# Kernel optimization log

Measured on AMD Instinct MI355X. Metric: run time of the kernel, lower is better.

Reference implementation:

```python
import jax, jax.numpy as jnp
import numpy as np

NUM_ROUTING = 3

def squash(s):
    # squash along the unit_size axis (axis=2), exactly as the torch module
    mag_sq = jnp.sum(s * s, axis=2, keepdims=True)
    mag = jnp.sqrt(mag_sq)
    return mag_sq / (1.0 + mag_sq) * (s / mag)

def setup_inputs() -> dict:
    key = jax.random.key(0)
    k1, k2 = jax.random.split(key)
    B, in_unit, in_channel = 512, 8, 1152
    num_unit, unit_size = 10, 16
    x = jax.random.normal(k1, (B, in_unit, in_channel), dtype=jnp.float32)
    weight = jax.random.normal(k2, (in_channel, num_unit, unit_size, in_unit), dtype=jnp.float32)
    return {"x": x, "weight": weight}

def reference(x, weight):
    B = x.shape[0]
    C, J = weight.shape[0], weight.shape[1]  # in_channel, num_unit
    xt = jnp.swapaxes(x, 1, 2)  # [B, C, in_unit]
    # u_hat[c, j, b, s] = W[c, j, s, :] @ x[b, c, :]
    u_hat = jnp.einsum('cjsi,bci->cjbs', weight, xt)  # [C, J, B, S]
    b_ij = jnp.zeros((C, J), dtype=x.dtype)
    v = None
    for _ in range(NUM_ROUTING):
        # DGL degree-bucketing puts all J capsule nodes in one bucket, so the
        # softmax(dim=0) in capsule_reduce is over the num_unit axis per input capsule
        c = jax.nn.softmax(b_ij, axis=1)          # [C, J]
        s = jnp.einsum('cj,cjbs->jbs', c, u_hat)  # [J, B, S]
        v = squash(s)                             # [J, B, S]
        # update_edge: b_ij += mean over batch of <v_j, u_hat_ij>
        b_ij = b_ij + jnp.einsum('jbs,cjbs->cj', v, u_hat) / B
    # [J, B, S] -> [B, J, S] -> unsqueeze(1).unsqueeze(4).squeeze(1) -> [B, J, S, 1]
    return jnp.transpose(v, (1, 0, 2))[..., None]
```

## Files before the change

kernel.cpp:

```cpp
#include <hip/hip_runtime.h>
#include <math.h>

#define B_  512
#define I_  8
#define C_  1152
#define J_  10
#define S_  16
#define K1  9216
#define NKB 288
#define KBT 16

typedef short short8 __attribute__((ext_vector_type(8)));
typedef float floatx4 __attribute__((ext_vector_type(4)));

__device__ inline unsigned short f2bf(float f) {
    unsigned int u = __float_as_uint(f);
    return (unsigned short)((u + 0x7FFFu + ((u >> 16) & 1u)) >> 16);
}
__device__ inline unsigned int pack2(float a, float b) {
    return (unsigned int)f2bf(a) | ((unsigned int)f2bf(b) << 16);
}

__global__ __launch_bounds__(512) void k_pack(const float* __restrict__ x,
                                              const float* __restrict__ W,
                                              uint4* __restrict__ Bs,
                                              uint4* __restrict__ Bt,
                                              uint4* __restrict__ Wf,
                                              unsigned short* __restrict__ W2,
                                              float* __restrict__ b_ij) {
    __shared__ float lds[10240];
    const int task = blockIdx.x;
    const int t = threadIdx.x;
    const int w = t >> 6, L = t & 63, quad = L >> 4;

    if (task < 576) {
        const int bt = task / 36, kt = task % 36;
        const int b0 = bt * 32, k0 = kt * 256;
        #pragma unroll
        for (int p = 0; p < 4; p++) {
            int f4 = p * 512 + t;
            int row = f4 >> 6, c4 = (f4 & 63) << 2;
            *(float4*)&lds[row * 260 + c4] =
                *(const float4*)&x[(size_t)(b0 + row) * K1 + k0 + c4];
        }
        __syncthreads();
        #pragma unroll
        for (int p = 0; p < 2; p++) {
            const int bl = p * 16 + (L & 15);
            const float* s = &lds[bl * 260 + w * 32 + quad * 8];
            uint4 o;
            o.x = pack2(s[0], s[1]); o.y = pack2(s[2], s[3]);
            o.z = pack2(s[4], s[5]); o.w = pack2(s[6], s[7]);
            Bs[((size_t)(bt * 2 + p) * NKB + kt * 8 + w) * 64 + L] = o;
        }
        #pragma unroll
        for (int p = 0; p < 2; p++) {
            const int ntl = w * 2 + p;
            const int nl = ntl * 16 + (L & 15);
            float v[8];
            #pragma unroll
            for (int e = 0; e < 8; e++) v[e] = lds[(quad * 8 + e) * 260 + nl];
            uint4 o;
            o.x = pack2(v[0], v[1]); o.y = pack2(v[2], v[3]);
            o.z = pack2(v[4], v[5]); o.w = pack2(v[6], v[7]);
            Bt[((size_t)(kt * 16 + ntl) * KBT + bt) * 64 + L] = o;
        }
    } else if (task < 720) {
        const int c0 = (task - 576) * 8;
        #pragma unroll
        for (int p = 0; p < 5; p++) {
            int f4 = p * 512 + t;
            int cc = f4 / 320, off4 = (f4 % 320) << 2;
            *(float4*)&lds[cc * 1280 + off4] =
                *(const float4*)&W[(size_t)(c0 + cc) * 1280 + off4];
        }
        __syncthreads();
        #pragma unroll
        for (int p = 0; p < 3; p++) {
            int o = p * 512 + t;
            if (o < 1280) {
                int j = o >> 7, i = (o >> 4) & 7, m = o & 15;
                int k0w = i * C_ + c0;
                int Lw = m | (((k0w >> 3) & 3) << 4);
                float v[8];
                #pragma unroll
                for (int e = 0; e < 8; e++)
                    v[e] = lds[e * 1280 + j * 128 + m * 8 + i];
                uint4 og;
                og.x = pack2(v[0], v[1]); og.y = pack2(v[2], v[3]);
                og.z = pack2(v[4], v[5]); og.w = pack2(v[6], v[7]);
                Wf[((size_t)j * NKB + (k0w >> 5)) * 64 + Lw] = og;
            }
        }
        #pragma unroll
        for (int p = 0; p < 2; p++) {
            int o = p * 512 + t;
            if (o < 640) {
                int j = o >> 6, i = (o >> 3) & 7, cc = o & 7;
                unsigned int r8[8];
                #pragma unroll
                for (int h = 0; h < 8; h++)
                    r8[h] = pack2(lds[cc * 1280 + j * 128 + (2 * h) * 8 + i],
                                  lds[cc * 1280 + j * 128 + (2 * h + 1) * 8 + i]);
                unsigned short* dst = W2 + ((size_t)(j * 8 + i) * C_ + c0 + cc) * 16;
                *(uint4*)dst       = make_uint4(r8[0], r8[1], r8[2], r8[3]);
                *(uint4*)(dst + 8) = make_uint4(r8[4], r8[5], r8[6], r8[7]);
            }
        }
    } else {
        for (int idx = t; idx < C_ * J_; idx += 512) b_ij[idx] = 0.0f;
    }
}

__global__ __launch_bounds__(256) void k_sgemm_f(const short8* __restrict__ Wf,
                                                 const short8* __restrict__ Bs,
                                                 const float* __restrict__ b_ij,
                                                 unsigned short* __restrict__ Vf,
                                                 float* __restrict__ out,
                                                 int mode) {
    __shared__ float sm[1152 + 2048];
    const int t = threadIdx.x, w = t >> 6, L = t & 63, quad = L >> 4;
    const int j = blockIdx.x >> 4;
    const int ntp = blockIdx.x & 15;

    if (mode) {
        for (int c = t; c < C_; c += 256) {
            float bv[J_], mx = -1e30f;
            #pragma unroll
            for (int jj = 0; jj < J_; jj++) {
                bv[jj] = b_ij[c * J_ + jj]; mx = fmaxf(mx, bv[jj]);
            }
            float sum = 0.0f;
            #pragma unroll
            for (int jj = 0; jj < J_; jj++) sum += __expf(bv[jj] - mx);
            sm[c] = __expf(bv[j] - mx) / sum;
        }
    }
    __syncthreads();

    const short8* pA  = Wf + ((size_t)j * NKB + w * 72) * 64 + L;
    const short8* pB0 = Bs + ((size_t)(ntp * 2) * NKB + w * 72) * 64 + L;
    const short8* pB1 = pB0 + (size_t)NKB * 64;
    floatx4 c0 = {0.f, 0.f, 0.f, 0.f}, c1 = c0;

    if (mode) {
        #pragma unroll 1
        for (int half = 0; half < 2; half++) {
            #pragma unroll 4
            for (int ii = 0; ii < 36; ii++) {
                const int i = half * 36 + ii;
                short8 a = pA[i * 64];
                const int cb = ii * 32 + quad * 8;
                float4 cl = *(const float4*)&sm[cb];
                float4 ch = *(const float4*)&sm[cb + 4];
                float cn8[8] = {cl.x, cl.y, cl.z, cl.w, ch.x, ch.y, ch.z, ch.w};
                unsigned int* au = (unsigned int*)&a;
                short8 a2;
                unsigned int* ao = (unsigned int*)&a2;
                #pragma unroll
                for (int h = 0; h < 4; h++) {
                    float f0 = __uint_as_float(au[h] << 16)         * cn8[2 * h];
                    float f1 = __uint_as_float(au[h] & 0xffff0000u) * cn8[2 * h + 1];
                    ao[h] = pack2(f0, f1);
                }
                c0 = __builtin_amdgcn_mfma_f32_16x16x32_bf16(a2, pB0[i * 64], c0, 0, 0, 0);
                c1 = __builtin_amdgcn_mfma_f32_16x16x32_bf16(a2, pB1[i * 64], c1, 0, 0, 0);
            }
        }
    } else {
        #pragma unroll 4
        for (int i = 0; i < 72; i++) {
            short8 a = pA[i * 64];
            c0 = __builtin_amdgcn_mfma_f32_16x16x32_bf16(a, pB0[i * 64], c0, 0, 0, 0);
            c1 = __builtin_amdgcn_mfma_f32_16x16x32_bf16(a, pB1[i * 64], c1, 0, 0, 0);
        }
    }

    const int col = L & 15, rw = quad << 2;
    float* base = &sm[1152 + w * 512];
    #pragma unroll
    for (int r = 0; r < 4; r++) {
        base[      (rw + r) * 16 + col] = c0[r];
        base[256 + (rw + r) * 16 + col] = c1[r];
    }
    __syncthreads();

    if (t < 32) {
        const int ntl = t >> 4, bl = t & 15;
        float sv[S_]; float msq = 0.f;
        #pragma unroll
        for (int s = 0; s < S_; s++) {
            float a = 0.f;
            #pragma unroll
            for (int w4 = 0; w4 < 4; w4++)
                a += sm[1152 + w4 * 512 + ntl * 256 + s * 16 + bl];
            if (mode == 0) a *= 0.1f;
            sv[s] = a; msq += a * a;
        }
        const float scale = msq / ((1.f + msq) * sqrtf(msq));
        const int b = ntp * 32 + t;
        if (mode < 2) {
            const int kb = b >> 5, lh = (b >> 3) & 3, e = b & 7;
            #pragma unroll
            for (int s = 0; s < S_; s++)
                Vf[((size_t)(j * KBT + kb) * 64 + (s | (lh << 4))) * 8 + e] =
                    f2bf(sv[s] * scale);
        } else {
            float o16[S_];
            #pragma unroll
            for (int s = 0; s < S_; s++) o16[s] = sv[s] * scale;
            float* dst = &out[((size_t)b * J_ + j) * S_];
            #pragma unroll
            for (int r4 = 0; r4 < 4; r4++)
                *(float4*)(dst + r4 * 4) = *(float4*)(o16 + r4 * 4);
        }
    }
}

__global__ __launch_bounds__(512) void k_tgemm_bup(const short8* __restrict__ Vf,
                                                   const short8* __restrict__ Bt,
                                                   const unsigned short* __restrict__ W2,
                                                   float* __restrict__ b_ij) {
    __shared__ float Tl[16 * 132];
    const int t = threadIdx.x, w = t >> 6, L = t & 63;
    const int j = blockIdx.y, ntg = blockIdx.x;
    const int nt = ntg * 8 + w;
    const short8* pA = Vf + (size_t)j * KBT * 64 + L;
    const short8* pB = Bt + (size_t)nt * KBT * 64 + L;
    floatx4 a = {0.f, 0.f, 0.f, 0.f};
    #pragma unroll
    for (int kb = 0; kb < KBT; kb++)
        a = __builtin_amdgcn_mfma_f32_16x16x32_bf16(pA[kb * 64], pB[kb * 64], a, 0, 0, 0);
    const int col = L & 15, rw = (L >> 4) << 2;
    #pragma unroll
    for (int r = 0; r < 4; r++)
        Tl[(rw + r) * 132 + w * 16 + col] = a[r];
    __syncthreads();
    if (t < 128) {
        const int n0 = ntg * 128;
        const int i = n0 / C_, c0 = n0 % C_;
        const int c = c0 + t;
        const unsigned short* wp = W2 + ((size_t)(j * 8 + i) * C_ + c) * 16;
        uint4 w0 = *(const uint4*)wp;
        uint4 w1 = *(const uint4*)(wp + 8);
        unsigned int uw[8] = {w0.x, w0.y, w0.z, w0.w, w1.x, w1.y, w1.z, w1.w};
        float sum = 0.f;
        #pragma unroll
        for (int h = 0; h < 8; h++) {
            sum += Tl[(2 * h) * 132 + t]     * __uint_as_float(uw[h] << 16);
            sum += Tl[(2 * h + 1) * 132 + t] * __uint_as_float(uw[h] & 0xffff0000u);
        }
        atomicAdd(&b_ij[c * J_ + j], sum * (1.0f / 512.f));
    }
}

extern "C" void kernel_launch(void* const* d_in, const int* in_sizes, int n_in,
                              void* d_out, int out_size, void* d_ws, size_t ws_size,
                              hipStream_t stream) {
    const float* x = (const float*)d_in[0];
    const float* W = (const float*)d_in[1];
    float* out = (float*)d_out;
    float* ws  = (float*)d_ws;

    float* Bs_f = ws;
    float* Bt_f = Bs_f + 2359296;
    float* Wf_f = Bt_f + 2359296;
    float* W2_f = Wf_f + 737280;
    float* Vf_f = W2_f + 737280;
    float* bij  = Vf_f + 40960;

    k_pack<<<721, 512, 0, stream>>>(x, W, (uint4*)Bs_f, (uint4*)Bt_f,
                                    (uint4*)Wf_f, (unsigned short*)W2_f, bij);

    k_sgemm_f<<<160, 256, 0, stream>>>((const short8*)Wf_f, (const short8*)Bs_f,
                                       bij, (unsigned short*)Vf_f, out, 0);
    k_tgemm_bup<<<dim3(72, 10), 512, 0, stream>>>(
        (const short8*)Vf_f, (const short8*)Bt_f, (const unsigned short*)W2_f, bij);

    k_sgemm_f<<<160, 256, 0, stream>>>((const short8*)Wf_f, (const short8*)Bs_f,
                                       bij, (unsigned short*)Vf_f, out, 1);
    k_tgemm_bup<<<dim3(72, 10), 512, 0, stream>>>(
        (const short8*)Vf_f, (const short8*)Bt_f, (const unsigned short*)W2_f, bij);

    k_sgemm_f<<<160, 256, 0, stream>>>((const short8*)Wf_f, (const short8*)Bs_f,
                                       bij, (unsigned short*)Vf_f, out, 2);
}
```

Baseline: 143.8 us.

## Fuse routing iterations into one persistent kernel with grid barriers

Replaces the five separate s-GEMM and t-GEMM/b-update launches with a single persistent kernel of 360 blocks. The blocks step through all routing phases and synchronise with a software grid barrier built on agent-scope atomics. The s-GEMM tiles are also re-split from 32 to 16 batch columns with 8 waves splitting K, which raises parallelism to 320 tasks. This removes launch gaps and gives more blocks in the first phase. In exchange it relies on all 360 blocks being co-resident, and the barrier uses a spin timeout that could silently break correctness if residency fails.

```diff
diff --git a/kernel.cpp b/kernel.cpp
--- a/kernel.cpp
+++ b/kernel.cpp
@@ -9,6 +9,8 @@
 #define K1  9216
 #define NKB 288
 #define KBT 16
+#define NBL 360
+#define NT  512
 
 typedef short short8 __attribute__((ext_vector_type(8)));
 typedef float floatx4 __attribute__((ext_vector_type(4)));
@@ -19,6 +21,27 @@
 }
 __device__ inline unsigned int pack2(float a, float b) {
     return (unsigned int)f2bf(a) | ((unsigned int)f2bf(b) << 16);
+}
+
+__device__ __forceinline__ void grid_bar(int* bar) {
+    __builtin_amdgcn_fence(__ATOMIC_RELEASE, "workgroup");
+    __syncthreads();
+    if (threadIdx.x == 0) {
+        int g = __hip_atomic_load(&bar[1], __ATOMIC_RELAXED, __HIP_MEMORY_SCOPE_AGENT);
+        int old = __hip_atomic_fetch_add(&bar[0], 1, __ATOMIC_RELAXED, __HIP_MEMORY_SCOPE_AGENT);
+        if (old == NBL - 1) {
+            __hip_atomic_store(&bar[0], 0, __ATOMIC_RELAXED, __HIP_MEMORY_SCOPE_AGENT);
+            __hip_atomic_store(&bar[1], g + 1, __ATOMIC_RELAXED, __HIP_MEMORY_SCOPE_AGENT);
+        } else {
+            int spins = 0;
+            while (__hip_atomic_load(&bar[1], __ATOMIC_RELAXED, __HIP_MEMORY_SCOPE_AGENT) == g) {
+                __builtin_amdgcn_s_sleep(1);
+                if (++spins > (1 << 20)) break;
+            }
+        }
+    }
+    __syncthreads();
+    __builtin_amdgcn_fence(__ATOMIC_ACQUIRE, "workgroup");
 }
 
 __global__ __launch_bounds__(512) void k_pack(const float* __restrict__ x,
@@ -27,7 +50,8 @@
                                               uint4* __restrict__ Bt,
                                               uint4* __restrict__ Wf,
                                               unsigned short* __restrict__ W2,
-                                              float* __restrict__ b_ij) {
+                                              float* __restrict__ b_ij,
+                                              int* __restrict__ bar) {
     __shared__ float lds[10240];
     const int task = blockIdx.x;
     const int t = threadIdx.x;
@@ -109,148 +133,153 @@
         }
     } else {
         for (int idx = t; idx < C_ * J_; idx += 512) b_ij[idx] = 0.0f;
+        if (t < 16) bar[t] = 0;
     }
 }
 
-__global__ __launch_bounds__(256) void k_sgemm_f(const short8* __restrict__ Wf,
-                                                 const short8* __restrict__ Bs,
-                                                 const float* __restrict__ b_ij,
-                                                 unsigned short* __restrict__ Vf,
-                                                 float* __restrict__ out,
-                                                 int mode) {
-    __shared__ float sm[1152 + 2048];
-    const int t = threadIdx.x, w = t >> 6, L = t & 63, quad = L >> 4;
-    const int j = blockIdx.x >> 4;
-    const int ntp = blockIdx.x & 15;
-
-    if (mode) {
-        for (int c = t; c < C_; c += 256) {
-            float bv[J_], mx = -1e30f;
+__global__ __launch_bounds__(NT, 4) void k_main(
+    const short8* __restrict__ Wf, const short8* __restrict__ Bs,
+    const short8* __restrict__ Bt, const unsigned short* __restrict__ W2,
+    unsigned int* __restrict__ Vf_dw, float* __restrict__ b_ij,
+    float* __restrict__ out, int* __restrict__ bar)
+{
+    __shared__ float smf[6400];
+    unsigned int* smu = (unsigned int*)smf;
+    const int bid = blockIdx.x, t = threadIdx.x;
+    const int w = t >> 6, L = t & 63, quad = L >> 4;
+
+    for (int it = 0; it < 3; it++) {
+        for (int task = bid; task < 320; task += NBL) {
+            __syncthreads();
+            const int j = task >> 5, nt = task & 31;
+            if (it > 0) {
+                for (int c = t; c < C_; c += NT) {
+                    float bv[J_], mx = -1e30f;
+                    #pragma unroll
+                    for (int jj = 0; jj < J_; jj++) {
+                        bv[jj] = __hip_atomic_load(&b_ij[c * J_ + jj],
+                                 __ATOMIC_RELAXED, __HIP_MEMORY_SCOPE_AGENT);
+                        mx = fmaxf(mx, bv[jj]);
+                    }
+                    float sum = 0.0f;
+                    #pragma unroll
+                    for (int jj = 0; jj < J_; jj++) sum += __expf(bv[jj] - mx);
+                    smf[c] = __expf(bv[j] - mx) / sum;
+                }
+            }
+            __syncthreads();
+            const short8* pA = Wf + ((size_t)j * NKB + w * 36) * 64 + L;
+            const short8* pB = Bs + ((size_t)nt * NKB + w * 36) * 64 + L;
+            floatx4 acc = {0.f, 0.f, 0.f, 0.f};
+            if (it > 0) {
+                #pragma unroll 4
+                for (int i = 0; i < 36; i++) {
+                    short8 a = pA[i * 64];
+                    const int cb = i * 32 + quad * 8;
+                    float4 cl = *(const float4*)&smf[cb];
+                    float4 ch = *(const float4*)&smf[cb + 4];
+                    float cn8[8] = {cl.x, cl.y, cl.z, cl.w, ch.x, ch.y, ch.z, ch.w};
+                    unsigned int* au = (unsigned int*)&a;
+                    short8 a2; unsigned int* ao = (unsigned int*)&a2;
+                    #pragma unroll
+                    for (int h = 0; h < 4; h++) {
+                        float f0 = __uint_as_float(au[h] << 16)         * cn8[2 * h];
+                        float f1 = __uint_as_float(au[h] & 0xffff0000u) * cn8[2 * h + 1];
+                        ao[h] = pack2(f0, f1);
+                    }
+                    acc = __builtin_amdgcn_mfma_f32_16x16x32_bf16(a2, pB[i * 64], acc, 0, 0, 0);
+                }
+            } else {
+                #pragma unroll 4
+                for (int i = 0; i < 36; i++)
+                    acc = __builtin_amdgcn_mfma_f32_16x16x32_bf16(pA[i * 64], pB[i * 64], acc, 0, 0, 0);
+            }
+            const int col = L & 15, rw = quad << 2;
             #pragma unroll
-            for (int jj = 0; jj < J_; jj++) {
-                bv[jj] = b_ij[c * J_ + jj]; mx = fmaxf(mx, bv[jj]);
-            }
-            float sum = 0.0f;
+            for (int r = 0; r < 4; r++)
+                smf[1152 + w * 256 + (rw + r) * 16 + col] = acc[r];
+            __syncthreads();
+            if (t < 16) {
+                float sv[S_]; float msq = 0.f;
+                #pragma unroll
+                for (int s = 0; s < S_; s++) {
+                    float a = 0.f;
+                    #pragma unroll
+                    for (int w8 = 0; w8 < 8; w8++)
+                        a += smf[1152 + w8 * 256 + s * 16 + t];
+                    if (it == 0) a *= 0.1f;
+                    sv[s] = a; msq += a * a;
+                }
+                const float scale = msq / ((1.f + msq) * sqrtf(msq));
+                if (it < 2) {
+                    #pragma unroll
+                    for (int s = 0; s < S_; s++)
+                        smf[3456 + t * 16 + s] = sv[s] * scale;
+                } else {
+                    const int b = nt * 16 + t;
+                    float o16[S_];
+                    #pragma unroll
+                    for (int s = 0; s < S_; s++) o16[s] = sv[s] * scale;
+                    float* dst = &out[((size_t)b * J_ + j) * S_];
+                    #pragma unroll
+                    for (int r4 = 0; r4 < 4; r4++)
+                        *(float4*)(dst + r4 * 4) = *(float4*)(o16 + r4 * 4);
+                }
+            }
+            if (it < 2 && t < 8) {
+                const int kb = nt >> 1;
+                const int e0 = (2 * t) & 7;
+                const int lh = ((nt & 1) << 1) | (t >> 2);
+                #pragma unroll
+                for (int s = 0; s < S_; s++) {
+                    unsigned int d = pack2(smf[3456 + (2 * t) * 16 + s],
+                                           smf[3456 + (2 * t + 1) * 16 + s]);
+                    int sidx = ((j * 16 + kb) * 64 + (s | (lh << 4))) * 8 + e0;
+                    __hip_atomic_store(&Vf_dw[sidx >> 1], d,
+                                       __ATOMIC_RELAXED, __HIP_MEMORY_SCOPE_AGENT);
+                }
+            }
+        }
+        if (it == 2) return;
+        grid_bar(bar);
+
+        for (int task = bid; task < 720; task += NBL) {
+            __syncthreads();
+            const int j = task / 72, ntg = task % 72;
+            for (int d = t; d < 4096; d += NT)
+                smu[d] = __hip_atomic_load(&Vf_dw[j * 4096 + d],
+                         __ATOMIC_RELAXED, __HIP_MEMORY_SCOPE_AGENT);
+            __syncthreads();
+            const int nt = ntg * 8 + w;
+            const short8* pB  = Bt + ((size_t)nt * KBT) * 64 + L;
+            const short8* pAl = (const short8*)smu + L;
+            floatx4 a = {0.f, 0.f, 0.f, 0.f};
             #pragma unroll
-            for (int jj = 0; jj < J_; jj++) sum += __expf(bv[jj] - mx);
-            sm[c] = __expf(bv[j] - mx) / sum;
-        }
-    }
-    __syncthreads();
-
-    const short8* pA  = Wf + ((size_t)j * NKB + w * 72) * 64 + L;
-    const short8* pB0 = Bs + ((size_t)(ntp * 2) * NKB + w * 72) * 64 + L;
-    const short8* pB1 = pB0 + (size_t)NKB * 64;
-    floatx4 c0 = {0.f, 0.f, 0.f, 0.f}, c1 = c0;
-
-    if (mode) {
-        #pragma unroll 1
-        for (int half = 0; half < 2; half++) {
-            #pragma unroll 4
-            for (int ii = 0; ii < 36; ii++) {
-                const int i = half * 36 + ii;
-                short8 a = pA[i * 64];
-                const int cb = ii * 32 + quad * 8;
-                float4 cl = *(const float4*)&sm[cb];
-                float4 ch = *(const float4*)&sm[cb + 4];
-                float cn8[8] = {cl.x, cl.y, cl.z, cl.w, ch.x, ch.y, ch.z, ch.w};
-                unsigned int* au = (unsigned int*)&a;
-                short8 a2;
-                unsigned int* ao = (unsigned int*)&a2;
-                #pragma unroll
-                for (int h = 0; h < 4; h++) {
-                    float f0 = __uint_as_float(au[h] << 16)         * cn8[2 * h];
-                    float f1 = __uint_as_float(au[h] & 0xffff0000u) * cn8[2 * h + 1];
-                    ao[h] = pack2(f0, f1);
-                }
-                c0 = __builtin_amdgcn_mfma_f32_16x16x32_bf16(a2, pB0[i * 64], c0, 0, 0, 0);
-                c1 = __builtin_amdgcn_mfma_f32_16x16x32_bf16(a2, pB1[i * 64], c1, 0, 0, 0);
-            }
-        }
-    } else {
-        #pragma unroll 4
-        for (int i = 0; i < 72; i++) {
-            short8 a = pA[i * 64];
-            c0 = __builtin_amdgcn_mfma_f32_16x16x32_bf16(a, pB0[i * 64], c0, 0, 0, 0);
-            c1 = __builtin_amdgcn_mfma_f32_16x16x32_bf16(a, pB1[i * 64], c1, 0, 0, 0);
-        }
-    }
-
-    const int col = L & 15, rw = quad << 2;
-    float* base = &sm[1152 + w * 512];
-    #pragma unroll
-    for (int r = 0; r < 4; r++) {
-        base[      (rw + r) * 16 + col] = c0[r];
-        base[256 + (rw + r) * 16 + col] = c1[r];
-    }
-    __syncthreads();
-
-    if (t < 32) {
-        const int ntl = t >> 4, bl = t & 15;
-        float sv[S_]; float msq = 0.f;
-        #pragma unroll
-        for (int s = 0; s < S_; s++) {
-            float a = 0.f;
+            for (int kb = 0; kb < KBT; kb++)
+                a = __builtin_amdgcn_mfma_f32_16x16x32_bf16(pAl[kb * 64], pB[kb * 64], a, 0, 0, 0);
+            const int col = L & 15, rw = quad << 2;
             #pragma unroll
-            for (int w4 = 0; w4 < 4; w4++)
-                a += sm[1152 + w4 * 512 + ntl * 256 + s * 16 + bl];
-            if (mode == 0) a *= 0.1f;
-            sv[s] = a; msq += a * a;
-        }
-        const float scale = msq / ((1.f + msq) * sqrtf(msq));
-        const int b = ntp * 32 + t;
-        if (mode < 2) {
-            const int kb = b >> 5, lh = (b >> 3) & 3, e = b & 7;
-            #pragma unroll
-            for (int s = 0; s < S_; s++)
-                Vf[((size_t)(j * KBT + kb) * 64 + (s | (lh << 4))) * 8 + e] =
-                    f2bf(sv[s] * scale);
-        } else {
-            float o16[S_];
-            #pragma unroll
-            for (int s = 0; s < S_; s++) o16[s] = sv[s] * scale;
-            float* dst = &out[((size_t)b * J_ + j) * S_];
-            #pragma unroll
-            for (int r4 = 0; r4 < 4; r4++)
-                *(float4*)(dst + r4 * 4) = *(float4*)(o16 + r4 * 4);
-        }
-    }
-}
-
-__global__ __launch_bounds__(512) void k_tgemm_bup(const short8* __restrict__ Vf,
-                                                   const short8* __restrict__ Bt,
-                                                   const unsigned short* __restrict__ W2,
-                                                   float* __restrict__ b_ij) {
-    __shared__ float Tl[16 * 132];
-    const int t = threadIdx.x, w = t >> 6, L = t & 63;
-    const int j = blockIdx.y, ntg = blockIdx.x;
-    const int nt = ntg * 8 + w;
-    const short8* pA = Vf + (size_t)j * KBT * 64 + L;
-    const short8* pB = Bt + (size_t)nt * KBT * 64 + L;
-    floatx4 a = {0.f, 0.f, 0.f, 0.f};
-    #pragma unroll
-    for (int kb = 0; kb < KBT; kb++)
-        a = __builtin_amdgcn_mfma_f32_16x16x32_bf16(pA[kb * 64], pB[kb * 64], a, 0, 0, 0);
-    const int col = L & 15, rw = (L >> 4) << 2;
-    #pragma unroll
-    for (int r = 0; r < 4; r++)
-        Tl[(rw + r) * 132 + w * 16 + col] = a[r];
-    __syncthreads();
-    if (t < 128) {
-        const int n0 = ntg * 128;
-        const int i = n0 / C_, c0 = n0 % C_;
-        const int c = c0 + t;
-        const unsigned short* wp = W2 + ((size_t)(j * 8 + i) * C_ + c) * 16;
-        uint4 w0 = *(const uint4*)wp;
-        uint4 w1 = *(const uint4*)(wp + 8);
-        unsigned int uw[8] = {w0.x, w0.y, w0.z, w0.w, w1.x, w1.y, w1.z, w1.w};
-        float sum = 0.f;
-        #pragma unroll
-        for (int h = 0; h < 8; h++) {
-            sum += Tl[(2 * h) * 132 + t]     * __uint_as_float(uw[h] << 16);
-            sum += Tl[(2 * h + 1) * 132 + t] * __uint_as_float(uw[h] & 0xffff0000u);
-        }
-        atomicAdd(&b_ij[c * J_ + j], sum * (1.0f / 512.f));
+            for (int r = 0; r < 4; r++)
+                smf[4096 + (rw + r) * 132 + w * 16 + col] = a[r];
+            __syncthreads();
+            if (t < 128) {
+                const int n0 = ntg * 128;
+                const int i = n0 / C_, c0 = n0 % C_;
+                const int c = c0 + t;
+                const unsigned short* wp = W2 + ((size_t)(j * 8 + i) * C_ + c) * 16;
+                uint4 w0 = *(const uint4*)wp;
+                uint4 w1 = *(const uint4*)(wp + 8);
+                unsigned int uw[8] = {w0.x, w0.y, w0.z, w0.w, w1.x, w1.y, w1.z, w1.w};
+                float sum = 0.f;
+                #pragma unroll
+                for (int h = 0; h < 8; h++) {
+                    sum += smf[4096 + (2 * h) * 132 + t]     * __uint_as_float(uw[h] << 16);
+                    sum += smf[4096 + (2 * h + 1) * 132 + t] * __uint_as_float(uw[h] & 0xffff0000u);
+                }
+                atomicAdd(&b_ij[c * J_ + j], sum * (1.0f / 512.f));
+            }
+        }
+        grid_bar(bar);
     }
 }
 
@@ -268,20 +297,12 @@
     float* W2_f = Wf_f + 737280;
     float* Vf_f = W2_f + 737280;
     float* bij  = Vf_f + 40960;
+    int*   bar  = (int*)(bij + 11520);
 
     k_pack<<<721, 512, 0, stream>>>(x, W, (uint4*)Bs_f, (uint4*)Bt_f,
-                                    (uint4*)Wf_f, (unsigned short*)W2_f, bij);
-
-    k_sgemm_f<<<160, 256, 0, stream>>>((const short8*)Wf_f, (const short8*)Bs_f,
-                                       bij, (unsigned short*)Vf_f, out, 0);
-    k_tgemm_bup<<<dim3(72, 10), 512, 0, stream>>>(
-        (const short8*)Vf_f, (const short8*)Bt_f, (const unsigned short*)W2_f, bij);
-
-    k_sgemm_f<<<160, 256, 0, stream>>>((const short8*)Wf_f, (const short8*)Bs_f,
-                                       bij, (unsigned short*)Vf_f, out, 1);
-    k_tgemm_bup<<<dim3(72, 10), 512, 0, stream>>>(
-        (const short8*)Vf_f, (const short8*)Bt_f, (const unsigned short*)W2_f, bij);
-
-    k_sgemm_f<<<160, 256, 0, stream>>>((const short8*)Wf_f, (const short8*)Bs_f,
-                                       bij, (unsigned short*)Vf_f, out, 2);
-}
+                                    (uint4*)Wf_f, (unsigned short*)W2_f, bij, bar);
+
+    k_main<<<NBL, NT, 0, stream>>>((const short8*)Wf_f, (const short8*)Bs_f,
+                                   (const short8*)Bt_f, (const unsigned short*)W2_f,
+                                   (unsigned int*)Vf_f, bij, out, bar);
+}
```

New measurement: 228.9 us. 59.1% more time.

## Double split-K waves in s-GEMM and reduce b_ij update with wave shuffles

Applied to the files above, without the earlier changes.

The s-GEMM kernel now launches 512 threads per block. Each of eight waves handles 36 K-blocks instead of 72, and the partial results are summed across eight slices in LDS. The b_ij update kernel drops its LDS staging, barrier and 128-thread serial dot product. Each wave instead multiplies its MFMA accumulator by the matching W2 entries, reduces with cross-lane shuffles, and issues atomics directly. This aims to cut serial latency in both small-grid kernels, at the cost of more LDS, a longer final reduction, and more atomics per output element.

```diff
diff --git a/kernel.cpp b/kernel.cpp
--- a/kernel.cpp
+++ b/kernel.cpp
@@ -112,19 +112,19 @@
     }
 }
 
-__global__ __launch_bounds__(256) void k_sgemm_f(const short8* __restrict__ Wf,
+__global__ __launch_bounds__(512) void k_sgemm_f(const short8* __restrict__ Wf,
                                                  const short8* __restrict__ Bs,
                                                  const float* __restrict__ b_ij,
                                                  unsigned short* __restrict__ Vf,
                                                  float* __restrict__ out,
                                                  int mode) {
-    __shared__ float sm[1152 + 2048];
+    __shared__ float smf[1152 + 4096];
     const int t = threadIdx.x, w = t >> 6, L = t & 63, quad = L >> 4;
     const int j = blockIdx.x >> 4;
     const int ntp = blockIdx.x & 15;
 
     if (mode) {
-        for (int c = t; c < C_; c += 256) {
+        for (int c = t; c < C_; c += 512) {
             float bv[J_], mx = -1e30f;
             #pragma unroll
             for (int jj = 0; jj < J_; jj++) {
@@ -133,43 +133,38 @@
             float sum = 0.0f;
             #pragma unroll
             for (int jj = 0; jj < J_; jj++) sum += __expf(bv[jj] - mx);
-            sm[c] = __expf(bv[j] - mx) / sum;
+            smf[c] = __expf(bv[j] - mx) / sum;
         }
     }
     __syncthreads();
 
-    const short8* pA  = Wf + ((size_t)j * NKB + w * 72) * 64 + L;
-    const short8* pB0 = Bs + ((size_t)(ntp * 2) * NKB + w * 72) * 64 + L;
+    const short8* pA  = Wf + ((size_t)j * NKB + w * 36) * 64 + L;
+    const short8* pB0 = Bs + ((size_t)(ntp * 2) * NKB + w * 36) * 64 + L;
     const short8* pB1 = pB0 + (size_t)NKB * 64;
     floatx4 c0 = {0.f, 0.f, 0.f, 0.f}, c1 = c0;
 
     if (mode) {
-        #pragma unroll 1
-        for (int half = 0; half < 2; half++) {
-            #pragma unroll 4
-            for (int ii = 0; ii < 36; ii++) {
-                const int i = half * 36 + ii;
-                short8 a = pA[i * 64];
-                const int cb = ii * 32 + quad * 8;
-                float4 cl = *(const float4*)&sm[cb];
-                float4 ch = *(const float4*)&sm[cb + 4];
-                float cn8[8] = {cl.x, cl.y, cl.z, cl.w, ch.x, ch.y, ch.z, ch.w};
-                unsigned int* au = (unsigned int*)&a;
-                short8 a2;
-                unsigned int* ao = (unsigned int*)&a2;
-                #pragma unroll
-                for (int h = 0; h < 4; h++) {
-                    float f0 = __uint_as_float(au[h] << 16)         * cn8[2 * h];
-                    float f1 = __uint_as_float(au[h] & 0xffff0000u) * cn8[2 * h + 1];
-                    ao[h] = pack2(f0, f1);
-                }
-                c0 = __builtin_amdgcn_mfma_f32_16x16x32_bf16(a2, pB0[i * 64], c0, 0, 0, 0);
-                c1 = __builtin_amdgcn_mfma_f32_16x16x32_bf16(a2, pB1[i * 64], c1, 0, 0, 0);
-            }
+        #pragma unroll 4
+        for (int i = 0; i < 36; i++) {
+            short8 a = pA[i * 64];
+            const int cb = i * 32 + quad * 8;
+            float4 cl = *(const float4*)&smf[cb];
+            float4 ch = *(const float4*)&smf[cb + 4];
+            float cn8[8] = {cl.x, cl.y, cl.z, cl.w, ch.x, ch.y, ch.z, ch.w};
+            unsigned int* au = (unsigned int*)&a;
+            short8 a2; unsigned int* ao = (unsigned int*)&a2;
+            #pragma unroll
+            for (int h = 0; h < 4; h++) {
+                float f0 = __uint_as_float(au[h] << 16)         * cn8[2 * h];
+                float f1 = __uint_as_float(au[h] & 0xffff0000u) * cn8[2 * h + 1];
+                ao[h] = pack2(f0, f1);
+            }
+            c0 = __builtin_amdgcn_mfma_f32_16x16x32_bf16(a2, pB0[i * 64], c0, 0, 0, 0);
+            c1 = __builtin_amdgcn_mfma_f32_16x16x32_bf16(a2, pB1[i * 64], c1, 0, 0, 0);
         }
     } else {
         #pragma unroll 4
-        for (int i = 0; i < 72; i++) {
+        for (int i = 0; i < 36; i++) {
             short8 a = pA[i * 64];
             c0 = __builtin_amdgcn_mfma_f32_16x16x32_bf16(a, pB0[i * 64], c0, 0, 0, 0);
             c1 = __builtin_amdgcn_mfma_f32_16x16x32_bf16(a, pB1[i * 64], c1, 0, 0, 0);
@@ -177,7 +172,7 @@
     }
 
     const int col = L & 15, rw = quad << 2;
-    float* base = &sm[1152 + w * 512];
+    float* base = &smf[1152 + w * 512];
     #pragma unroll
     for (int r = 0; r < 4; r++) {
         base[      (rw + r) * 16 + col] = c0[r];
@@ -192,8 +187,8 @@
         for (int s = 0; s < S_; s++) {
             float a = 0.f;
             #pragma unroll
-            for (int w4 = 0; w4 < 4; w4++)
-                a += sm[1152 + w4 * 512 + ntl * 256 + s * 16 + bl];
+            for (int w8 = 0; w8 < 8; w8++)
+                a += smf[1152 + w8 * 512 + ntl * 256 + s * 16 + bl];
             if (mode == 0) a *= 0.1f;
             sv[s] = a; msq += a * a;
         }
@@ -221,7 +216,6 @@
                                                    const short8* __restrict__ Bt,
                                                    const unsigned short* __restrict__ W2,
                                                    float* __restrict__ b_ij) {
-    __shared__ float Tl[16 * 132];
     const int t = threadIdx.x, w = t >> 6, L = t & 63;
     const int j = blockIdx.y, ntg = blockIdx.x;
     const int nt = ntg * 8 + w;
@@ -232,26 +226,18 @@
     for (int kb = 0; kb < KBT; kb++)
         a = __builtin_amdgcn_mfma_f32_16x16x32_bf16(pA[kb * 64], pB[kb * 64], a, 0, 0, 0);
     const int col = L & 15, rw = (L >> 4) << 2;
-    #pragma unroll
-    for (int r = 0; r < 4; r++)
-        Tl[(rw + r) * 132 + w * 16 + col] = a[r];
-    __syncthreads();
-    if (t < 128) {
-        const int n0 = ntg * 128;
-        const int i = n0 / C_, c0 = n0 % C_;
-        const int c = c0 + t;
-        const unsigned short* wp = W2 + ((size_t)(j * 8 + i) * C_ + c) * 16;
-        uint4 w0 = *(const uint4*)wp;
-        uint4 w1 = *(const uint4*)(wp + 8);
-        unsigned int uw[8] = {w0.x, w0.y, w0.z, w0.w, w1.x, w1.y, w1.z, w1.w};
-        float sum = 0.f;
-        #pragma unroll
-        for (int h = 0; h < 8; h++) {
-            sum += Tl[(2 * h) * 132 + t]     * __uint_as_float(uw[h] << 16);
-            sum += Tl[(2 * h + 1) * 132 + t] * __uint_as_float(uw[h] & 0xffff0000u);
-        }
-        atomicAdd(&b_ij[c * J_ + j], sum * (1.0f / 512.f));
-    }
+    const int i = nt / 72;
+    const int c = (nt % 72) * 16 + col;
+    const unsigned short* wp = W2 + ((size_t)(j * 8 + i) * C_ + c) * 16 + rw;
+    uint2 wv = *(const uint2*)wp;
+    float p = a[0] * __uint_as_float((unsigned int)wv.x << 16)
+            + a[1] * __uint_as_float(wv.x & 0xffff0000u)
+            + a[2] * __uint_as_float((unsigned int)wv.y << 16)
+            + a[3] * __uint_as_float(wv.y & 0xffff0000u);
+    p += __shfl_xor(p, 16);
+    p += __shfl_xor(p, 32);
+    if ((L >> 4) == 0)
+        atomicAdd(&b_ij[c * J_ + j], p * (1.0f / 512.f));
 }
 
 extern "C" void kernel_launch(void* const* d_in, const int* in_sizes, int n_in,
@@ -272,16 +258,16 @@
     k_pack<<<721, 512, 0, stream>>>(x, W, (uint4*)Bs_f, (uint4*)Bt_f,
                                     (uint4*)Wf_f, (unsigned short*)W2_f, bij);
 
-    k_sgemm_f<<<160, 256, 0, stream>>>((const short8*)Wf_f, (const short8*)Bs_f,
+    k_sgemm_f<<<160, 512, 0, stream>>>((const short8*)Wf_f, (const short8*)Bs_f,
                                        bij, (unsigned short*)Vf_f, out, 0);
     k_tgemm_bup<<<dim3(72, 10), 512, 0, stream>>>(
         (const short8*)Vf_f, (const short8*)Bt_f, (const unsigned short*)W2_f, bij);
 
-    k_sgemm_f<<<160, 256, 0, stream>>>((const short8*)Wf_f, (const short8*)Bs_f,
+    k_sgemm_f<<<160, 512, 0, stream>>>((const short8*)Wf_f, (const short8*)Bs_f,
                                        bij, (unsigned short*)Vf_f, out, 1);
     k_tgemm_bup<<<dim3(72, 10), 512, 0, stream>>>(
         (const short8*)Vf_f, (const short8*)Bt_f, (const unsigned short*)W2_f, bij);
 
-    k_sgemm_f<<<160, 256, 0, stream>>>((const short8*)Wf_f, (const short8*)Bs_f,
+    k_sgemm_f<<<160, 512, 0, stream>>>((const short8*)Wf_f, (const short8*)Bs_f,
                                        bij, (unsigned short*)Vf_f, out, 2);
 }
```

Result: no change. 143.0 us (-0.6%).
